# Kernel optimization log

Measured on AMD Instinct MI355X. Metric: run time of the kernel, lower is better.

## Reference

```python
import jax, jax.numpy as jnp
import numpy as np

P = 8          # patch_size
HEADS = 4      # patch_size // 2
DIM = 256      # nf*P*P // 16
DH = DIM // HEADS


def setup_inputs() -> dict:
    key = jax.random.key(0)
    ks = jax.random.split(key, 8)
    B, N, C, H, W = 8, 1, 64, 256, 256
    Np = (H // P) * (W // P)           # 1024
    patch_dim = C * P * P              # 4096
    s = 0.02
    return {
        "x": jax.random.normal(ks[0], (B, N, C, H, W), jnp.float32),
        "W_embed": jax.random.normal(ks[1], (DIM, patch_dim), jnp.float32) * s,
        "b_embed": jnp.zeros((DIM,), jnp.float32),
        "pos": jax.random.normal(ks[2], (1, Np, DIM), jnp.float32),
        "Wq": jax.random.normal(ks[3], (DIM, DIM), jnp.float32) * s,
        "Wk": jax.random.normal(ks[4], (Np, Np), jnp.float32) * s,
        "Wv": jax.random.normal(ks[5], (DIM, DIM), jnp.float32) * s,
        "Wout": jax.random.normal(ks[6], (patch_dim, DIM), jnp.float32) * s,
        "b_out": jnp.zeros((patch_dim,), jnp.float32),
    }


def reference(x, W_embed, b_embed, pos, Wq, Wk, Wv, Wout, b_out):
    B, N, C, H, W = x.shape
    Hp, Wp = H // P, W // P
    Np = Hp * Wp
    patch_dim = C * P * P
    BN = B * N

    # unfold (non-overlapping patches), column order = (C, kh, kw)
    xb = x.reshape(BN, C, Hp, P, Wp, P)
    patches = xb.transpose(0, 2, 4, 1, 3, 5).reshape(BN, Np, patch_dim)

    # linear_embed + positional embedding
    emb = jnp.einsum('bnp,dp->bnd', patches, W_embed) + b_embed + pos  # (BN, Np, DIM)

    # q: linear, split heads, mean over head-dim (AvgPool1d(dh) on length dh)
    q = jnp.einsum('bnd,ed->bne', emb, Wq)
    q = q.reshape(BN, Np, HEADS, DH).transpose(0, 2, 1, 3)  # (BN, H, Np, DH)
    q = q.mean(axis=-1)                                      # (BN, H, Np)

    # k = sigmoid(linear_k(q)); diag_embed(k) @ v == k[..., None] * v
    k = jax.nn.sigmoid(jnp.einsum('bhn,mn->bhm', q, Wk))     # (BN, H, Np)

    v = jnp.einsum('bnd,ed->bne', emb, Wv)
    v = v.reshape(BN, Np, HEADS, DH).transpose(0, 2, 1, 3)   # (BN, H, Np, DH)

    out = k[..., None] * v                                   # (BN, H, Np, DH)
    out = out.transpose(0, 2, 1, 3).reshape(BN, Np, DIM)

    out = jnp.einsum('bnd,pd->bnp', out, Wout) + b_out       # (BN, Np, patch_dim)

    # fold back to image
    out = out.reshape(BN, Hp, Wp, C, P, P).transpose(0, 3, 1, 4, 2, 5)
    out = out.reshape(B, N, C, H, W)
    return out
```

## Files before the change

kernel.cpp:

```cpp
#include <hip/hip_runtime.h>

typedef __attribute__((ext_vector_type(8))) short short8;
typedef __attribute__((ext_vector_type(4))) float f32x4;

#define LDA 72
#define KST 260

__device__ __forceinline__ unsigned short f2bf(float f) {
  unsigned int u = __builtin_bit_cast(unsigned int, f);
  u += 0x7fffu + ((u >> 16) & 1u);
  return (unsigned short)(u >> 16);
}
__device__ __forceinline__ float bf2f(unsigned short us) {
  return __builtin_bit_cast(float, (unsigned int)us << 16);
}

__device__ __forceinline__ short8 cvt8(float4 lo, float4 hi) {
  short8 v;
  v[0] = (short)f2bf(lo.x); v[1] = (short)f2bf(lo.y);
  v[2] = (short)f2bf(lo.z); v[3] = (short)f2bf(lo.w);
  v[4] = (short)f2bf(hi.x); v[5] = (short)f2bf(hi.y);
  v[6] = (short)f2bf(hi.z); v[7] = (short)f2bf(hi.w);
  return v;
}

__device__ __forceinline__ void mfma_tile(const unsigned short* __restrict__ Ab,
                                          const unsigned short* __restrict__ Bb,
                                          int wm, int wn, int lr, int lq,
                                          f32x4 (&acc)[2][4]) {
#pragma unroll
  for (int kc = 0; kc < 2; ++kc) {
    short8 a0 = *(const short8*)&Ab[(wm * 32 + lr) * LDA + kc * 32 + lq * 8];
    short8 a1 = *(const short8*)&Ab[(wm * 32 + 16 + lr) * LDA + kc * 32 + lq * 8];
#pragma unroll
    for (int ni = 0; ni < 4; ++ni) {
      short8 b = *(const short8*)&Bb[(wn * 64 + ni * 16 + lr) * LDA + kc * 32 + lq * 8];
      acc[0][ni] = __builtin_amdgcn_mfma_f32_16x16x32_bf16(a0, b, acc[0][ni], 0, 0, 0);
      acc[1][ni] = __builtin_amdgcn_mfma_f32_16x16x32_bf16(a1, b, acc[1][ni], 0, 0, 0);
    }
  }
}

__device__ __forceinline__ void cvt_block(const float* __restrict__ src,
                                          unsigned short* __restrict__ dst, int b) {
  int i = b * 256 + threadIdx.x;
  float4 f = ((const float4*)src)[i];
  unsigned int lo = (unsigned int)f2bf(f.x) | ((unsigned int)f2bf(f.y) << 16);
  unsigned int hi = (unsigned int)f2bf(f.z) | ((unsigned int)f2bf(f.w) << 16);
  uint2 u; u.x = lo; u.y = hi;
  ((uint2*)dst)[i] = u;
}

__global__ __launch_bounds__(256) void prep_kernel(
    const float* __restrict__ W_embed, const float* __restrict__ Wout,
    const float* __restrict__ Wv, const float* __restrict__ Wq,
    unsigned short* __restrict__ Wb, unsigned short* __restrict__ Wob,
    unsigned short* __restrict__ Wvb, float* __restrict__ WqR) {
  int b = blockIdx.x;
  if (b < 1024) { cvt_block(W_embed, Wb, b); return; }
  if (b < 2048) { cvt_block(Wout, Wob, b - 1024); return; }
  if (b < 2112) { cvt_block(Wv, Wvb, b - 2048); return; }
  int idx = (b - 2112) * 256 + threadIdx.x;
  int h = idx >> 8, e = idx & 255;
  float s = 0.f;
  for (int j = 0; j < 64; ++j) s += Wq[(size_t)(h * 64 + j) * 256 + e];
  WqR[idx] = s * (1.f / 64.f);
}

struct StageV3 { float4 a0, a1; short8 b[8]; };

__global__ __launch_bounds__(256, 1) void gemm1_fused(
    const float* __restrict__ x, const unsigned short* __restrict__ Wb,
    const float* __restrict__ b_embed, const float* __restrict__ pos,
    const float* __restrict__ WqR,
    unsigned short* __restrict__ emb_bf, float* __restrict__ q) {
  __shared__ __align__(16) unsigned short lds[41472];
  __shared__ float wq_s[1024];
  unsigned short* A0 = lds;
  unsigned short* A1 = lds + 2304;
  unsigned short* B0 = lds + 4608;
  unsigned short* B1 = lds + 23040;
  float* esm = (float*)(lds + 4608);

  const int t = threadIdx.x;
  const int wave = t >> 6, lane = t & 63;
  const int wn = wave;
  const int lr = lane & 15, lq = lane >> 4;
  const int m0 = blockIdx.x * 32;
  const int bn = m0 >> 10;
  const int nbase = m0 & 1023;
  const int ph = nbase >> 5;

  for (int i = t; i < 1024; i += 256) wq_s[i] = WqR[i];

  const int mA = t >> 3, kc8 = t & 7;
  const float* pa = x + ((size_t)(bn << 6) << 16) +
                    (size_t)((ph << 3) + kc8) * 256 + (mA << 3);
  const int dA = mA * LDA + (kc8 << 3);
  const unsigned short* pb = Wb + (size_t)(t >> 3) * 4096 + ((t & 7) << 3);
  const int dB = (t >> 3) * LDA + ((t & 7) << 3);

  f32x4 acc[2][4];
#pragma unroll
  for (int i = 0; i < 2; i++)
#pragma unroll
    for (int j = 0; j < 4; j++) acc[i][j] = f32x4{0.f, 0.f, 0.f, 0.f};

  StageV3 st0, st1;
#define G1F_LOAD(st, kt)                                                         \
  {                                                                              \
    const float* qa = pa + (size_t)(kt) * 65536;                                 \
    st.a0 = *(const float4*)qa; st.a1 = *(const float4*)(qa + 4);                \
    _Pragma("unroll")                                                            \
    for (int i = 0; i < 8; ++i)                                                  \
      st.b[i] = *(const short8*)(pb + (size_t)i * 131072 + (kt) * 64);           \
  }
#define G1F_WRITE(st, Aw, Bw)                                                    \
  {                                                                              \
    *(short8*)&Aw[dA] = cvt8(st.a0, st.a1);                                      \
    _Pragma("unroll")                                                            \
    for (int i = 0; i < 8; ++i) *(short8*)&Bw[dB + i * 32 * LDA] = st.b[i];      \
  }

  G1F_LOAD(st0, 0)
  G1F_LOAD(st1, 1)
  G1F_WRITE(st0, A0, B0)
  __syncthreads();

#pragma unroll 1
  for (int p = 0; p < 31; ++p) {
    G1F_LOAD(st0, 2 * p + 2)
    mfma_tile(A0, B0, 0, wn, lr, lq, acc);
    G1F_WRITE(st1, A1, B1)
    __syncthreads();
    G1F_LOAD(st1, 2 * p + 3)
    mfma_tile(A1, B1, 0, wn, lr, lq, acc);
    G1F_WRITE(st0, A0, B0)
    __syncthreads();
  }
  mfma_tile(A0, B0, 0, wn, lr, lq, acc);
  G1F_WRITE(st1, A1, B1)
  __syncthreads();
  mfma_tile(A1, B1, 0, wn, lr, lq, acc);

#pragma unroll
  for (int mi = 0; mi < 2; ++mi)
#pragma unroll
    for (int ni = 0; ni < 4; ++ni) {
      int col = wn * 64 + ni * 16 + lr;
      int rb = mi * 16 + lq * 4;
#pragma unroll
      for (int r2 = 0; r2 < 4; ++r2)
        esm[(rb + r2) * 264 + col] = acc[mi][ni][r2];
    }
  __syncthreads();

  {
    const int row = t >> 3, seg = t & 7;
    const int n = nbase + row;
    const float4* e4 = (const float4*)esm;
    const float4* b4 = (const float4*)b_embed;
    const float4* pos4 = (const float4*)pos;
    const float4* wq4 = (const float4*)wq_s;
    float4 e[8];
#pragma unroll
    for (int j = 0; j < 8; ++j) {
      float4 v = e4[row * 66 + seg * 8 + j];
      float4 bb = b4[seg * 8 + j];
      float4 pp = pos4[(size_t)n * 64 + seg * 8 + j];
      e[j].x = v.x + bb.x + pp.x;
      e[j].y = v.y + bb.y + pp.y;
      e[j].z = v.z + bb.z + pp.z;
      e[j].w = v.w + bb.w + pp.w;
    }
    unsigned int ub[16];
#pragma unroll
    for (int j = 0; j < 8; ++j) {
      ub[2 * j]     = (unsigned int)f2bf(e[j].x) | ((unsigned int)f2bf(e[j].y) << 16);
      ub[2 * j + 1] = (unsigned int)f2bf(e[j].z) | ((unsigned int)f2bf(e[j].w) << 16);
    }
    uint4* dst = (uint4*)(emb_bf + (size_t)(m0 + row) * 256 + seg * 32);
#pragma unroll
    for (int j = 0; j < 4; ++j)
      dst[j] = make_uint4(ub[4 * j], ub[4 * j + 1], ub[4 * j + 2], ub[4 * j + 3]);
    float s[4] = {0.f, 0.f, 0.f, 0.f};
#pragma unroll
    for (int h = 0; h < 4; ++h)
#pragma unroll
      for (int j = 0; j < 8; ++j) {
        float4 w = wq4[h * 64 + seg * 8 + j];
        s[h] += e[j].x * w.x + e[j].y * w.y + e[j].z * w.z + e[j].w * w.w;
      }
#pragma unroll
    for (int h = 0; h < 4; ++h) {
      s[h] += __shfl_xor(s[h], 1);
      s[h] += __shfl_xor(s[h], 2);
      s[h] += __shfl_xor(s[h], 4);
    }
    if (seg == 0) {
#pragma unroll
      for (int h = 0; h < 4; ++h)
        q[(size_t)(bn * 4 + h) * 1024 + n] = s[h];
    }
  }
#undef G1F_LOAD
#undef G1F_WRITE
}

__global__ __launch_bounds__(256) void k_kernel(const float* __restrict__ q,
                                                const float* __restrict__ Wk,
                                                float* __restrict__ kk) {
  __shared__ float wk_s[8 * KST];
  __shared__ float q_s[32 * KST];
  const int m0 = blockIdx.x * 8;
  const int t = threadIdx.x;
  const int m = t & 7, bh = t >> 3;
  const float4* wkg = (const float4*)Wk;
  const float4* qg = (const float4*)q;
  float acc = 0.f;
  for (int kt = 0; kt < 4; ++kt) {
    const int k0 = kt * 256;
#pragma unroll
    for (int i = 0; i < 2; ++i) {
      int idx = t + i * 256;
      int r = idx >> 6, c4 = idx & 63;
      *(float4*)&wk_s[r * KST + c4 * 4] = wkg[((size_t)(m0 + r) * 1024 + k0) / 4 + c4];
    }
#pragma unroll
    for (int i = 0; i < 8; ++i) {
      int idx = t + i * 256;
      int r = idx >> 6, c4 = idx & 63;
      *(float4*)&q_s[r * KST + c4 * 4] = qg[((size_t)r * 1024 + k0) / 4 + c4];
    }
    __syncthreads();
#pragma unroll 8
    for (int k4 = 0; k4 < 64; ++k4) {
      float4 a = *(const float4*)&wk_s[m * KST + k4 * 4];
      float4 b = *(const float4*)&q_s[bh * KST + k4 * 4];
      acc += a.x * b.x + a.y * b.y + a.z * b.z + a.w * b.w;
    }
    __syncthreads();
  }
  kk[(size_t)bh * 1024 + m0 + m] = 1.f / (1.f + __expf(-acc));
}

#define VST 264
__global__ __launch_bounds__(256) void vgemm_kernel(
    const unsigned short* __restrict__ Abf, const unsigned short* __restrict__ Wvb,
    const float* __restrict__ kk, unsigned short* __restrict__ ov) {
  __shared__ __align__(16) unsigned short Vs[128 * VST];
  const int nt = blockIdx.x, mt = blockIdx.y;
  const int m0 = mt * 64, n0 = nt * 64;
  const int t = threadIdx.x;
  const int wave = t >> 6, lane = t & 63;
  const int wr = wave >> 1, wc = wave & 1;
  const int lr = lane & 15, lq = lane >> 4;

  const int row0 = t >> 5, kb = t & 31;
#pragma unroll
  for (int i = 0; i < 8; ++i)
    *(short8*)&Vs[(row0 + i * 8) * VST + kb * 8] =
        *(const short8*)(Abf + (size_t)(m0 + row0 + i * 8) * 256 + kb * 8);
#pragma unroll
  for (int i = 0; i < 8; ++i)
    *(short8*)&Vs[(64 + row0 + i * 8) * VST + kb * 8] =
        *(const short8*)(Wvb + (size_t)(n0 + row0 + i * 8) * 256 + kb * 8);
  __syncthreads();

  f32x4 acc[2][2];
#pragma unroll
  for (int i = 0; i < 2; ++i)
#pragma unroll
    for (int j = 0; j < 2; ++j) acc[i][j] = f32x4{0.f, 0.f, 0.f, 0.f};

#pragma unroll
  for (int kc = 0; kc < 8; ++kc) {
    short8 a0 = *(const short8*)&Vs[(wr * 32 + lr) * VST + kc * 32 + lq * 8];
    short8 a1 = *(const short8*)&Vs[(wr * 32 + 16 + lr) * VST + kc * 32 + lq * 8];
    short8 b0 = *(const short8*)&Vs[(64 + wc * 32 + lr) * VST + kc * 32 + lq * 8];
    short8 b1 = *(const short8*)&Vs[(64 + wc * 32 + 16 + lr) * VST + kc * 32 + lq * 8];
    acc[0][0] = __builtin_amdgcn_mfma_f32_16x16x32_bf16(a0, b0, acc[0][0], 0, 0, 0);
    acc[0][1] = __builtin_amdgcn_mfma_f32_16x16x32_bf16(a0, b1, acc[0][1], 0, 0, 0);
    acc[1][0] = __builtin_amdgcn_mfma_f32_16x16x32_bf16(a1, b0, acc[1][0], 0, 0, 0);
    acc[1][1] = __builtin_amdgcn_mfma_f32_16x16x32_bf16(a1, b1, acc[1][1], 0, 0, 0);
  }

#pragma unroll
  for (int mi = 0; mi < 2; ++mi)
#pragma unroll
    for (int ni = 0; ni < 2; ++ni) {
      int col = n0 + wc * 32 + ni * 16 + lr;
      int h = col >> 6;
      int rbase = m0 + wr * 32 + mi * 16 + lq * 4;
#pragma unroll
      for (int r2 = 0; r2 < 4; ++r2) {
        int row = rbase + r2;
        int bn = row >> 10, n = row & 1023;
        float g = kk[(size_t)(bn * 4 + h) * 1024 + n];
        ov[(size_t)row * 256 + col] = f2bf(acc[mi][ni][r2] * g);
      }
    }
}

#define CST 132
struct StageG2 { short8 a[2]; short8 b[4]; };

__device__ __forceinline__ void g2_load(StageG2& s, const unsigned short* pA,
                                        const unsigned short* pB, int k0) {
#pragma unroll
  for (int i = 0; i < 2; ++i)
    s.a[i] = *(const short8*)(pA + (size_t)i * 32 * 256 + k0);
#pragma unroll
  for (int i = 0; i < 4; ++i)
    s.b[i] = *(const short8*)(pB + (size_t)i * 32 * 256 + k0);
}
__device__ __forceinline__ void g2_write(unsigned short* Ab, unsigned short* Bb,
                                         int dA, int dB, const StageG2& s) {
#pragma unroll
  for (int i = 0; i < 2; ++i) *(short8*)&Ab[dA + i * 32 * LDA] = s.a[i];
#pragma unroll
  for (int i = 0; i < 4; ++i) *(short8*)&Bb[dB + i * 32 * LDA] = s.b[i];
}

__global__ __launch_bounds__(256, 2) void gemm2_out(
    const unsigned short* __restrict__ Abf, const unsigned short* __restrict__ Wob,
    const float* __restrict__ b_out, float* __restrict__ out) {
  __shared__ __align__(16) unsigned short smbuf[2][192 * LDA];
  float* csm = (float*)&smbuf[0][0];
  const int nt = blockIdx.x, mt = blockIdx.y;
  const int m0 = mt * 64, n0 = nt * 128;
  const int t = threadIdx.x;
  const int wave = t >> 6, lane = t & 63;
  const int wm = wave >> 1, wn = wave & 1;
  const int lr = lane & 15, lq = lane >> 4;

  unsigned short* A0 = &smbuf[0][0]; unsigned short* B0 = &smbuf[0][64 * LDA];
  unsigned short* A1 = &smbuf[1][0]; unsigned short* B1 = &smbuf[1][64 * LDA];

  const unsigned short* pA = Abf + (size_t)(m0 + (t >> 3)) * 256 + (t & 7) * 8;
  const unsigned short* pB = Wob + (size_t)(n0 + (t >> 3)) * 256 + (t & 7) * 8;
  const int dA = (t >> 3) * LDA + (t & 7) * 8;
  const int dB = dA;

  f32x4 acc[2][4];
#pragma unroll
  for (int i = 0; i < 2; i++)
#pragma unroll
    for (int j = 0; j < 4; j++) acc[i][j] = f32x4{0.f, 0.f, 0.f, 0.f};

  StageG2 st0, st1;
  g2_load(st0, pA, pB, 0);
  g2_load(st1, pA, pB, 64);
  g2_write(A0, B0, dA, dB, st0);
  __syncthreads();
  g2_load(st0, pA, pB, 128);
  mfma_tile(A0, B0, wm, wn, lr, lq, acc);
  g2_write(A1, B1, dA, dB, st1);
  __syncthreads();
  g2_load(st1, pA, pB, 192);
  mfma_tile(A1, B1, wm, wn, lr, lq, acc);
  g2_write(A0, B0, dA, dB, st0);
  __syncthreads();
  mfma_tile(A0, B0, wm, wn, lr, lq, acc);
  g2_write(A1, B1, dA, dB, st1);
  __syncthreads();
  mfma_tile(A1, B1, wm, wn, lr, lq, acc);
  __syncthreads();

#pragma unroll
  for (int mi = 0; mi < 2; ++mi)
#pragma unroll
    for (int ni = 0; ni < 4; ++ni) {
      int pl = wn * 64 + ni * 16 + lr;
      int mb = wm * 32 + mi * 16 + lq * 4;
#pragma unroll
      for (int r2 = 0; r2 < 4; ++r2)
        csm[(mb + r2) * CST + pl] = acc[mi][ni][r2];
    }
  __syncthreads();
  const int bn = m0 >> 10;
  const int ph0 = (m0 & 1023) >> 5;
  const int c0 = n0 >> 6;
#pragma unroll
  for (int i = 0; i < 8; ++i) {
    int idx4 = t + i * 256;
    int kw4 = idx4 & 1;
    int pw = (idx4 >> 1) & 31;
    int kh = (idx4 >> 6) & 7;
    int c2 = (idx4 >> 9) & 1;
    int ph = (idx4 >> 10) & 1;
    int m_local = ph * 32 + pw;
    int p_local = c2 * 64 + kh * 8 + kw4 * 4;
    float4 v = *(const float4*)&csm[m_local * CST + p_local];
    float4 bo = *(const float4*)(b_out + n0 + p_local);
    v.x += bo.x; v.y += bo.y; v.z += bo.z; v.w += bo.w;
    size_t addr = ((size_t)((bn << 6) + c0 + c2) << 16) +
                  (size_t)(((ph0 + ph) << 3) + kh) * 256 + (pw << 3) + kw4 * 4;
    *(float4*)(out + addr) = v;
  }
}

extern "C" void kernel_launch(void* const* d_in, const int* in_sizes, int n_in,
                              void* d_out, int out_size, void* d_ws, size_t ws_size,
                              hipStream_t stream) {
  const float* x       = (const float*)d_in[0];
  const float* W_embed = (const float*)d_in[1];
  const float* b_embed = (const float*)d_in[2];
  const float* pos     = (const float*)d_in[3];
  const float* Wq      = (const float*)d_in[4];
  const float* Wk      = (const float*)d_in[5];
  const float* Wv      = (const float*)d_in[6];
  const float* Wout    = (const float*)d_in[7];
  const float* b_out   = (const float*)d_in[8];
  float* out = (float*)d_out;

  char* ws = (char*)d_ws;
  const size_t MB = 1024 * 1024;
  unsigned short* emb_bf = (unsigned short*)(ws);
  unsigned short* ov     = (unsigned short*)(ws + 4 * MB);
  unsigned short* Wb     = (unsigned short*)(ws + 8 * MB);
  unsigned short* Wob    = (unsigned short*)(ws + 10 * MB);
  unsigned short* Wvb    = (unsigned short*)(ws + 12 * MB);
  float* q               = (float*)(ws + 12 * MB + 131072);
  float* kk              = (float*)(ws + 12 * MB + 262144);
  float* WqR             = (float*)(ws + 12 * MB + 393216);

  prep_kernel<<<2116, 256, 0, stream>>>(W_embed, Wout, Wv, Wq, Wb, Wob, Wvb, WqR);
  gemm1_fused<<<256, 256, 0, stream>>>(x, Wb, b_embed, pos, WqR, emb_bf, q);
  k_kernel<<<128, 256, 0, stream>>>(q, Wk, kk);
  vgemm_kernel<<<dim3(4, 128), 256, 0, stream>>>(emb_bf, Wvb, kk, ov);
  gemm2_out<<<dim3(32, 128), 256, 0, stream>>>(ov, Wob, b_out, out);
}
```

Before: 323.2 us.

## Restructure embed GEMM to 512 threads with B operands loaded directly to registers

```diff
diff --git a/kernel.cpp b/kernel.cpp
--- a/kernel.cpp
+++ b/kernel.cpp
@@ -67,87 +67,101 @@
   WqR[idx] = s * (1.f / 64.f);
 }
 
-struct StageV3 { float4 a0, a1; short8 b[8]; };
-
-__global__ __launch_bounds__(256, 1) void gemm1_fused(
+__global__ __launch_bounds__(512, 2) void gemm1_fused(
     const float* __restrict__ x, const unsigned short* __restrict__ Wb,
     const float* __restrict__ b_embed, const float* __restrict__ pos,
     const float* __restrict__ WqR,
     unsigned short* __restrict__ emb_bf, float* __restrict__ q) {
-  __shared__ __align__(16) unsigned short lds[41472];
+  __shared__ __align__(16) unsigned short As[2][32 * LDA];
+  __shared__ __align__(16) float esm[32 * 264];
   __shared__ float wq_s[1024];
-  unsigned short* A0 = lds;
-  unsigned short* A1 = lds + 2304;
-  unsigned short* B0 = lds + 4608;
-  unsigned short* B1 = lds + 23040;
-  float* esm = (float*)(lds + 4608);
 
   const int t = threadIdx.x;
   const int wave = t >> 6, lane = t & 63;
-  const int wn = wave;
   const int lr = lane & 15, lq = lane >> 4;
   const int m0 = blockIdx.x * 32;
   const int bn = m0 >> 10;
   const int nbase = m0 & 1023;
   const int ph = nbase >> 5;
 
-  for (int i = t; i < 1024; i += 256) wq_s[i] = WqR[i];
-
-  const int mA = t >> 3, kc8 = t & 7;
+  for (int i = t; i < 1024; i += 512) wq_s[i] = WqR[i];
+
+  const int mA = t >> 4;
+  const int kh_ = (t & 15) >> 1, kw0 = (t & 1) * 4;
   const float* pa = x + ((size_t)(bn << 6) << 16) +
-                    (size_t)((ph << 3) + kc8) * 256 + (mA << 3);
-  const int dA = mA * LDA + (kc8 << 3);
-  const unsigned short* pb = Wb + (size_t)(t >> 3) * 4096 + ((t & 7) << 3);
-  const int dB = (t >> 3) * LDA + ((t & 7) << 3);
-
-  f32x4 acc[2][4];
-#pragma unroll
-  for (int i = 0; i < 2; i++)
-#pragma unroll
-    for (int j = 0; j < 4; j++) acc[i][j] = f32x4{0.f, 0.f, 0.f, 0.f};
-
-  StageV3 st0, st1;
-#define G1F_LOAD(st, kt)                                                         \
-  {                                                                              \
-    const float* qa = pa + (size_t)(kt) * 65536;                                 \
-    st.a0 = *(const float4*)qa; st.a1 = *(const float4*)(qa + 4);                \
-    _Pragma("unroll")                                                            \
-    for (int i = 0; i < 8; ++i)                                                  \
-      st.b[i] = *(const short8*)(pb + (size_t)i * 131072 + (kt) * 64);           \
-  }
-#define G1F_WRITE(st, Aw, Bw)                                                    \
-  {                                                                              \
-    *(short8*)&Aw[dA] = cvt8(st.a0, st.a1);                                      \
-    _Pragma("unroll")                                                            \
-    for (int i = 0; i < 8; ++i) *(short8*)&Bw[dB + i * 32 * LDA] = st.b[i];      \
-  }
-
-  G1F_LOAD(st0, 0)
-  G1F_LOAD(st1, 1)
-  G1F_WRITE(st0, A0, B0)
+                    (size_t)((ph << 3) + kh_) * 256 + (mA << 3) + kw0;
+  const int dA = mA * LDA + (t & 15) * 4;
+
+  const unsigned short* pB = Wb + (size_t)(wave * 32 + lr) * 4096 + lq * 8;
+
+  f32x4 acc[2][2];
+#pragma unroll
+  for (int i = 0; i < 2; ++i)
+#pragma unroll
+    for (int j = 0; j < 2; ++j) acc[i][j] = f32x4{0.f, 0.f, 0.f, 0.f};
+
+  float4 st0, st1;
+  short8 bcur[2][2], bnxt[2][2];
+
+#define G1F_ALOAD(st, kt) { st = *(const float4*)(pa + (size_t)(kt) * 65536); }
+#define G1F_AWRITE(st, buf)                                                     \
+  {                                                                             \
+    unsigned int w0 = (unsigned int)f2bf(st.x) | ((unsigned int)f2bf(st.y) << 16); \
+    unsigned int w1 = (unsigned int)f2bf(st.z) | ((unsigned int)f2bf(st.w) << 16); \
+    uint2 u; u.x = w0; u.y = w1;                                                \
+    *(uint2*)&As[buf][dA] = u;                                                  \
+  }
+#define G1F_BLOAD(bf, kt)                                                       \
+  {                                                                             \
+    _Pragma("unroll")                                                           \
+    for (int ni = 0; ni < 2; ++ni)                                              \
+      _Pragma("unroll")                                                         \
+      for (int kc = 0; kc < 2; ++kc)                                            \
+        bf[ni][kc] = *(const short8*)(pB + ni * 65536 + (kt) * 64 + kc * 32);   \
+  }
+#define G1F_MFMA(buf, bf)                                                       \
+  {                                                                             \
+    _Pragma("unroll")                                                           \
+    for (int kc = 0; kc < 2; ++kc) {                                            \
+      short8 a0 = *(const short8*)&As[buf][lr * LDA + kc * 32 + lq * 8];        \
+      short8 a1 = *(const short8*)&As[buf][(16 + lr) * LDA + kc * 32 + lq * 8]; \
+      acc[0][0] = __builtin_amdgcn_mfma_f32_16x16x32_bf16(a0, bf[0][kc], acc[0][0], 0, 0, 0); \
+      acc[0][1] = __builtin_amdgcn_mfma_f32_16x16x32_bf16(a0, bf[1][kc], acc[0][1], 0, 0, 0); \
+      acc[1][0] = __builtin_amdgcn_mfma_f32_16x16x32_bf16(a1, bf[0][kc], acc[1][0], 0, 0, 0); \
+      acc[1][1] = __builtin_amdgcn_mfma_f32_16x16x32_bf16(a1, bf[1][kc], acc[1][1], 0, 0, 0); \
+    }                                                                           \
+  }
+
+  G1F_ALOAD(st0, 0)
+  G1F_ALOAD(st1, 1)
+  G1F_BLOAD(bcur, 0)
+  G1F_AWRITE(st0, 0)
   __syncthreads();
 
 #pragma unroll 1
   for (int p = 0; p < 31; ++p) {
-    G1F_LOAD(st0, 2 * p + 2)
-    mfma_tile(A0, B0, 0, wn, lr, lq, acc);
-    G1F_WRITE(st1, A1, B1)
+    G1F_ALOAD(st0, 2 * p + 2)
+    G1F_BLOAD(bnxt, 2 * p + 1)
+    G1F_MFMA(0, bcur)
+    G1F_AWRITE(st1, 1)
     __syncthreads();
-    G1F_LOAD(st1, 2 * p + 3)
-    mfma_tile(A1, B1, 0, wn, lr, lq, acc);
-    G1F_WRITE(st0, A0, B0)
+    G1F_ALOAD(st1, 2 * p + 3)
+    G1F_BLOAD(bcur, 2 * p + 2)
+    G1F_MFMA(1, bnxt)
+    G1F_AWRITE(st0, 0)
     __syncthreads();
   }
-  mfma_tile(A0, B0, 0, wn, lr, lq, acc);
-  G1F_WRITE(st1, A1, B1)
-  __syncthreads();
-  mfma_tile(A1, B1, 0, wn, lr, lq, acc);
+  G1F_BLOAD(bnxt, 63)
+  G1F_MFMA(0, bcur)
+  G1F_AWRITE(st1, 1)
+  __syncthreads();
+  G1F_MFMA(1, bnxt)
 
 #pragma unroll
   for (int mi = 0; mi < 2; ++mi)
 #pragma unroll
-    for (int ni = 0; ni < 4; ++ni) {
-      int col = wn * 64 + ni * 16 + lr;
+    for (int ni = 0; ni < 2; ++ni) {
+      int col = wave * 32 + ni * 16 + lr;
       int rb = mi * 16 + lq * 4;
 #pragma unroll
       for (int r2 = 0; r2 < 4; ++r2)
@@ -156,39 +170,38 @@
   __syncthreads();
 
   {
-    const int row = t >> 3, seg = t & 7;
+    const int row = t >> 4, seg = t & 15;
     const int n = nbase + row;
     const float4* e4 = (const float4*)esm;
     const float4* b4 = (const float4*)b_embed;
     const float4* pos4 = (const float4*)pos;
     const float4* wq4 = (const float4*)wq_s;
-    float4 e[8];
-#pragma unroll
-    for (int j = 0; j < 8; ++j) {
-      float4 v = e4[row * 66 + seg * 8 + j];
-      float4 bb = b4[seg * 8 + j];
-      float4 pp = pos4[(size_t)n * 64 + seg * 8 + j];
+    float4 e[4];
+#pragma unroll
+    for (int j = 0; j < 4; ++j) {
+      float4 v = e4[row * 66 + seg * 4 + j];
+      float4 bb = b4[seg * 4 + j];
+      float4 pp = pos4[(size_t)n * 64 + seg * 4 + j];
       e[j].x = v.x + bb.x + pp.x;
       e[j].y = v.y + bb.y + pp.y;
       e[j].z = v.z + bb.z + pp.z;
       e[j].w = v.w + bb.w + pp.w;
     }
-    unsigned int ub[16];
-#pragma unroll
-    for (int j = 0; j < 8; ++j) {
+    unsigned int ub[8];
+#pragma unroll
+    for (int j = 0; j < 4; ++j) {
       ub[2 * j]     = (unsigned int)f2bf(e[j].x) | ((unsigned int)f2bf(e[j].y) << 16);
       ub[2 * j + 1] = (unsigned int)f2bf(e[j].z) | ((unsigned int)f2bf(e[j].w) << 16);
     }
-    uint4* dst = (uint4*)(emb_bf + (size_t)(m0 + row) * 256 + seg * 32);
-#pragma unroll
-    for (int j = 0; j < 4; ++j)
-      dst[j] = make_uint4(ub[4 * j], ub[4 * j + 1], ub[4 * j + 2], ub[4 * j + 3]);
+    uint4* dst = (uint4*)(emb_bf + (size_t)(m0 + row) * 256 + seg * 16);
+    dst[0] = make_uint4(ub[0], ub[1], ub[2], ub[3]);
+    dst[1] = make_uint4(ub[4], ub[5], ub[6], ub[7]);
     float s[4] = {0.f, 0.f, 0.f, 0.f};
 #pragma unroll
     for (int h = 0; h < 4; ++h)
 #pragma unroll
-      for (int j = 0; j < 8; ++j) {
-        float4 w = wq4[h * 64 + seg * 8 + j];
+      for (int j = 0; j < 4; ++j) {
+        float4 w = wq4[h * 64 + seg * 4 + j];
         s[h] += e[j].x * w.x + e[j].y * w.y + e[j].z * w.z + e[j].w * w.w;
       }
 #pragma unroll
@@ -196,6 +209,7 @@
       s[h] += __shfl_xor(s[h], 1);
       s[h] += __shfl_xor(s[h], 2);
       s[h] += __shfl_xor(s[h], 4);
+      s[h] += __shfl_xor(s[h], 8);
     }
     if (seg == 0) {
 #pragma unroll
@@ -203,8 +217,10 @@
         q[(size_t)(bn * 4 + h) * 1024 + n] = s[h];
     }
   }
-#undef G1F_LOAD
-#undef G1F_WRITE
+#undef G1F_ALOAD
+#undef G1F_AWRITE
+#undef G1F_BLOAD
+#undef G1F_MFMA
 }
 
 __global__ __launch_bounds__(256) void k_kernel(const float* __restrict__ q,
@@ -426,7 +442,7 @@
   float* WqR             = (float*)(ws + 12 * MB + 393216);
 
   prep_kernel<<<2116, 256, 0, stream>>>(W_embed, Wout, Wv, Wq, Wb, Wob, Wvb, WqR);
-  gemm1_fused<<<256, 256, 0, stream>>>(x, Wb, b_embed, pos, WqR, emb_bf, q);
+  gemm1_fused<<<256, 512, 0, stream>>>(x, Wb, b_embed, pos, WqR, emb_bf, q);
   k_kernel<<<128, 256, 0, stream>>>(q, Wk, kk);
   vgemm_kernel<<<dim3(4, 128), 256, 0, stream>>>(emb_bf, Wvb, kk, ov);
   gemm2_out<<<dim3(32, 128), 256, 0, stream>>>(ov, Wob, b_out, out);
```

Measured after the change: 324.7 us. About the same (+0.5%).
